# Kernel optimization log

Measured on AMD Instinct MI355X. Metric: run time of the kernel, lower is better.

## Reference

```python
import jax, jax.numpy as jnp
import numpy as np

N = 262144
HID = 200


def _lin_init(k, out_d, in_d):
    k1, k2 = jax.random.split(k)
    bound = 1.0 / np.sqrt(in_d)
    W = jax.random.uniform(k1, (out_d, in_d), minval=-bound, maxval=bound, dtype=jnp.float32)
    b = jax.random.uniform(k2, (out_d,), minval=-bound, maxval=bound, dtype=jnp.float32)
    return W, b


def setup_inputs() -> dict:
    key = jax.random.key(0)
    ks = jax.random.split(key, 10)
    Wu0, bu0 = _lin_init(ks[0], HID, 3)
    Wu1, bu1 = _lin_init(ks[1], HID, HID)
    Wu2, bu2 = _lin_init(ks[2], 1, HID)
    Wv0, bv0 = _lin_init(ks[3], HID, 3)
    Wv1, bv1 = _lin_init(ks[4], HID, HID)
    Wv2, bv2 = _lin_init(ks[5], 1, HID)
    Wf0, bf0 = _lin_init(ks[6], HID, 12)
    Wf1, bf1 = _lin_init(ks[7], HID, HID)
    Wf2, bf2 = _lin_init(ks[8], 2, HID)
    inputs = jax.random.normal(ks[9], (N, 3), dtype=jnp.float32)
    return dict(inputs=inputs,
                Wu0=Wu0, bu0=bu0, Wu1=Wu1, bu1=bu1, Wu2=Wu2, bu2=bu2,
                Wv0=Wv0, bv0=bv0, Wv1=Wv1, bv1=bv1, Wv2=Wv2, bv2=bv2,
                Wf0=Wf0, bf0=bf0, Wf1=Wf1, bf1=bf1, Wf2=Wf2, bf2=bf2)


def _mlp(x, W0, b0, W1, b1, W2, b2):
    # NN with num_layers=3: sin(Linear) -> sin(Linear) -> Linear
    h = jnp.sin(x @ W0.T + b0)
    h = jnp.sin(h @ W1.T + b1)
    return h @ W2.T + b2


def _scalar(pt, params):
    # per-point scalar network, pt: [3]
    W0, b0, W1, b1, W2, b2 = params
    h = jnp.sin(W0 @ pt + b0)
    h = jnp.sin(W1 @ h + b1)
    return (W2 @ h + b2)[0]


def _derivs(pt, params):
    # first derivatives (grad) and diagonal second derivatives u_xx, u_yy
    # via forward-over-reverse (jvp of grad) with unit tangents e_x, e_y.
    g = jax.grad(lambda p: _scalar(p, params))
    ex = jnp.array([1.0, 0.0, 0.0], dtype=pt.dtype)
    ey = jnp.array([0.0, 1.0, 0.0], dtype=pt.dtype)
    grad, hx = jax.jvp(g, (pt,), (ex,))
    _, hy = jax.jvp(g, (pt,), (ey,))
    return grad, hx[0], hy[1]


def _dhpm_forward(inputs, pu, pv, pf):
    u = _mlp(inputs, *pu)  # [N,1]
    v = _mlp(inputs, *pv)  # [N,1]
    gu, u_xx, u_yy = jax.vmap(lambda p: _derivs(p, pu))(inputs)
    gv, v_xx, v_yy = jax.vmap(lambda p: _derivs(p, pv))(inputs)
    u_x, u_y, u_t = gu[:, :1], gu[:, 1:2], gu[:, 2:3]
    v_x, v_y, v_t = gv[:, :1], gv[:, 1:2], gv[:, 2:3]
    u_xx = u_xx[:, None]; u_yy = u_yy[:, None]
    v_xx = v_xx[:, None]; v_yy = v_yy[:, None]
    feat = jnp.concatenate([u, v, u_t, v_t, u_x, u_xx, u_y, u_yy,
                            v_x, v_xx, v_y, v_yy], axis=1)  # [N,12]
    f = _mlp(feat, *pf)  # [N,2]
    return (u, v, u_t, v_t, u_x, u_xx, u_y, u_yy,
            v_x, v_xx, v_y, v_yy, f[:, :1], f[:, 1:])


def reference(inputs, Wu0, bu0, Wu1, bu1, Wu2, bu2,
              Wv0, bv0, Wv1, bv1, Wv2, bv2,
              Wf0, bf0, Wf1, bf1, Wf2, bf2):
    pu = (Wu0, bu0, Wu1, bu1, Wu2, bu2)
    pv = (Wv0, bv0, Wv1, bv1, Wv2, bv2)
    pf = (Wf0, bf0, Wf1, bf1, Wf2, bf2)
    return _dhpm_forward(inputs, pu, pv, pf)
```

## Files before the change

kernel.cpp:

```cpp
#include <hip/hip_runtime.h>


#define HID 200
#define NT 13
#define KT 7
#define BLDK 232
#define WCHUNK 8192
#define NTH 512
#define ELD 68

#define OFF_WU 0
#define OFF_WV 106496
#define OFF_WF 212992
#define OFF_CU 319488
#define OFF_CV 322688
#define OFF_CF 325888

typedef _Float16 f16;
typedef _Float16 f16x2 __attribute__((ext_vector_type(2)));
typedef _Float16 f16x8 __attribute__((ext_vector_type(8)));
typedef float f32x4 __attribute__((ext_vector_type(4)));

#define GLDS16(gp, lp) __builtin_amdgcn_global_load_lds( \
    (const __attribute__((address_space(1))) void*)(gp), \
    (__attribute__((address_space(3))) void*)(lp), 16, 0, 0)

__global__ __launch_bounds__(256) void dhpm_prep(
    const float* __restrict__ Wu1, const float* __restrict__ Wv1, const float* __restrict__ Wf1,
    const float* __restrict__ Wu0, const float* __restrict__ bu0,
    const float* __restrict__ Wv0, const float* __restrict__ bv0,
    const float* __restrict__ Wf0, const float* __restrict__ bf0,
    char* __restrict__ ws)
{
    int id = blockIdx.x * blockDim.x + threadIdx.x;
    const int nW = 3 * NT * 16 * 116;
    if (id < nW) {
        const int net = id / (NT*16*116);
        int e = id - net * (NT*16*116);
        const int nt  = e / (16*116);  e -= nt * (16*116);
        const int row = e / 116;
        const int k2  = e - row * 116;
        const int j   = nt*16 + row;
        const int k   = k2*2;
        const float* W = (net == 0) ? Wu1 : (net == 1) ? Wv1 : Wf1;
        f16x2 v; v[0] = (f16)0.f; v[1] = (f16)0.f;
        if (j < HID) {
            if (k     < HID) v[0] = (f16)W[j*HID + k];
            if (k + 1 < HID) v[1] = (f16)W[j*HID + k + 1];
        }
        *(f16x2*)(ws + net*106496 + nt*WCHUNK + row*464 + k2*4) = v;
        return;
    }
    id -= nW;
    if (id < 400) {
        const int net = id / HID;
        const int r   = id - net*HID;
        const float* W0 = net ? Wv0 : Wu0;
        const float* b0 = net ? bv0 : bu0;
        float4 c;
        c.x = W0[r*3+0]; c.y = W0[r*3+1]; c.z = W0[r*3+2]; c.w = b0[r];
        *(float4*)(ws + (net ? OFF_CV : OFF_CU) + r*16) = c;
        return;
    }
    id -= 400;
    if (id < HID) {
        const int i = id;
        float4 c0, c1, c2, c3;
        c0.x = Wf0[i*12+0];  c0.y = Wf0[i*12+1];  c0.z = Wf0[i*12+2];  c0.w = Wf0[i*12+3];
        c1.x = Wf0[i*12+4];  c1.y = Wf0[i*12+5];  c1.z = Wf0[i*12+6];  c1.w = Wf0[i*12+7];
        c2.x = Wf0[i*12+8];  c2.y = Wf0[i*12+9];  c2.z = Wf0[i*12+10]; c2.w = Wf0[i*12+11];
        c3.x = bf0[i]; c3.y = 0.f; c3.z = 0.f; c3.w = 0.f;
        char* p = ws + OFF_CF + i*64;
        *(float4*)(p)      = c0;
        *(float4*)(p + 16) = c1;
        *(float4*)(p + 32) = c2;
        *(float4*)(p + 48) = c3;
    }
}

__device__ __forceinline__ f32x4 mfma16(f16x8 a, f16x8 b, f32x4 c) {
    return __builtin_amdgcn_mfma_f32_16x16x32_f16(a, b, c, 0, 0, 0);
}

__device__ __forceinline__ void run_net(
    const float* __restrict__ inp, const char* __restrict__ ws,
    const int wOff, const int cstOff,
    const float* __restrict__ b1, const float* __restrict__ W2, const float b2s,
    const int cV, const int cXX, const int cYY,
    const int cX, const int cY, const int cT,
    char* __restrict__ Bb0, char* __restrict__ Bb1,
    float* __restrict__ exch, float* __restrict__ res,
    const int gp0, const int lane, const int w, const int q, const int g,
    const int jl, const int klo)
{
    const char* src = ws + wOff;

    GLDS16(src + w*1024 + lane*16, Bb0 + w*1024);

    f16x8 aP[3][KT];
    {
        const float4* cst = (const float4*)(ws + cstOff);
        const int pt = gp0 + q*16 + jl;
        const float x = inp[pt*3+0], y = inp[pt*3+1], tt = inp[pt*3+2];
        #pragma unroll
        for (int kt = 0; kt < KT; ++kt) {
            f16x8 f0, f1, f2;
            #pragma unroll
            for (int e = 0; e < 8; ++e) {
                const int i = kt*32 + klo*8 + e;
                const float4 c = cst[(i < HID) ? i : 0];
                const float z = fmaf(c.x, x, fmaf(c.y, y, fmaf(c.z, tt, c.w)));
                if (g == 0) {
                    const float s = __sinf(z);
                    f0[e] = (f16)s;
                    f1[e] = (f16)(-s * c.x * c.x);
                    f2[e] = (f16)(-s * c.y * c.y);
                } else {
                    const float cv = __cosf(z);
                    f0[e] = (f16)(cv * c.x);
                    f1[e] = (f16)(cv * c.y);
                    f2[e] = (f16)(cv * c.z);
                }
            }
            aP[0][kt] = f0; aP[1][kt] = f1; aP[2][kt] = f2;
        }
    }

    float p0a[4] = {0,0,0,0}, p1a[4] = {0,0,0,0}, p2a[4] = {0,0,0,0};

    float* E0  = exch;
    float* Edx = exch + 16*ELD;
    float* Edy = exch + 32*ELD;

    __syncthreads();

    for (int nt = 0; nt < NT; ++nt) {
        const char* Bcur = (nt & 1) ? Bb1 : Bb0;
        char*       Bnxt = (nt & 1) ? Bb0 : Bb1;
        if (nt + 1 < NT)
            GLDS16(src + (nt+1)*WCHUNK + w*1024 + lane*16, Bnxt + w*1024);

        f32x4 acc0 = {0,0,0,0}, acc1 = {0,0,0,0}, acc2 = {0,0,0,0};
        const f16* BH = (const f16*)Bcur;
        #pragma unroll
        for (int kt = 0; kt < KT; ++kt) {
            const f16x8 b = *(const f16x8*)&BH[jl*BLDK + kt*32 + klo*8];
            acc0 = mfma16(aP[0][kt], b, acc0);
            acc1 = mfma16(aP[1][kt], b, acc1);
            acc2 = mfma16(aP[2][kt], b, acc2);
        }

        const int j = nt*16 + jl;
        const float b1j = (j < HID) ? b1[j] : 0.f;
        const float w2j = (j < HID) ? W2[j] : 0.f;
        const int pcol = q*16 + klo*4;
        float wcr[4], wsr[4];
        if (g == 0) {
            f32x4 wc4;
            #pragma unroll
            for (int r = 0; r < 4; ++r) {
                float s1, c1;
                __sincosf(acc0[r] + b1j, &s1, &c1);
                wcr[r] = w2j * c1;
                wsr[r] = w2j * s1;
                p0a[r] += wsr[r];
                wc4[r] = wcr[r];
            }
            *(f32x4*)&E0[jl*ELD + pcol] = wc4;
        } else {
            *(f32x4*)&Edx[jl*ELD + pcol] = acc0;
            *(f32x4*)&Edy[jl*ELD + pcol] = acc1;
        }
        __syncthreads();

        if (g == 0) {
            const f32x4 ydx = *(const f32x4*)&Edx[jl*ELD + pcol];
            const f32x4 ydy = *(const f32x4*)&Edy[jl*ELD + pcol];
            #pragma unroll
            for (int r = 0; r < 4; ++r) {
                p1a[r] = fmaf(wcr[r], acc1[r], fmaf(-wsr[r]*ydx[r], ydx[r], p1a[r]));
                p2a[r] = fmaf(wcr[r], acc2[r], fmaf(-wsr[r]*ydy[r], ydy[r], p2a[r]));
            }
        } else {
            const f32x4 wc4 = *(const f32x4*)&E0[jl*ELD + pcol];
            #pragma unroll
            for (int r = 0; r < 4; ++r) {
                p0a[r] = fmaf(wc4[r], acc0[r], p0a[r]);
                p1a[r] = fmaf(wc4[r], acc1[r], p1a[r]);
                p2a[r] = fmaf(wc4[r], acc2[r], p2a[r]);
            }
        }
        __syncthreads();
    }

    #pragma unroll
    for (int d = 1; d < 16; d <<= 1)
        #pragma unroll
        for (int r = 0; r < 4; ++r) {
            p0a[r] += __shfl_xor(p0a[r], d);
            p1a[r] += __shfl_xor(p1a[r], d);
            p2a[r] += __shfl_xor(p2a[r], d);
        }
    if (jl == 0) {
        const int p0 = q*16 + klo*4;
        f32x4 v;
        if (g == 0) {
            #pragma unroll
            for (int r = 0; r < 4; ++r) v[r] = p0a[r] + b2s;
            *(f32x4*)&res[cV*72 + p0] = v;
            #pragma unroll
            for (int r = 0; r < 4; ++r) v[r] = p1a[r];
            *(f32x4*)&res[cXX*72 + p0] = v;
            #pragma unroll
            for (int r = 0; r < 4; ++r) v[r] = p2a[r];
            *(f32x4*)&res[cYY*72 + p0] = v;
        } else {
            #pragma unroll
            for (int r = 0; r < 4; ++r) v[r] = p0a[r];
            *(f32x4*)&res[cX*72 + p0] = v;
            #pragma unroll
            for (int r = 0; r < 4; ++r) v[r] = p1a[r];
            *(f32x4*)&res[cY*72 + p0] = v;
            #pragma unroll
            for (int r = 0; r < 4; ++r) v[r] = p2a[r];
            *(f32x4*)&res[cT*72 + p0] = v;
        }
    }
}

__global__ __launch_bounds__(NTH, 2) void dhpm_main(
    const float* __restrict__ inp, const char* __restrict__ ws,
    const float* __restrict__ bu1, const float* __restrict__ Wu2, const float* __restrict__ bu2,
    const float* __restrict__ bv1, const float* __restrict__ Wv2, const float* __restrict__ bv2,
    const float* __restrict__ bf1, const float* __restrict__ Wf2, const float* __restrict__ bf2,
    float* __restrict__ out, const int Np)
{
    __shared__ __align__(16) char LDS[37824];
    char*  Bb0  = LDS;
    char*  Bb1  = LDS + 8192;
    float* exch = (float*)(LDS + 16384);
    f16*   Af   = (f16*)LDS;
    float* res  = (float*)(LDS + 29696);
    float* pfb  = (float*)(LDS + 33728);

    const int t = threadIdx.x;
    const int lane = t & 63;
    const int w = __builtin_amdgcn_readfirstlane(t >> 6);
    const int q = w & 3, g = w >> 2;
    const int jl = lane & 15, klo = lane >> 4;
    const int gp0 = blockIdx.x * 64;

    run_net(inp, ws, OFF_WU, OFF_CU, bu1, Wu2, bu2[0], 0, 5, 7, 4, 6, 2,
            Bb0, Bb1, exch, res, gp0, lane, w, q, g, jl, klo);
    run_net(inp, ws, OFF_WV, OFF_CV, bv1, Wv2, bv2[0], 1, 9, 11, 8, 10, 3,
            Bb0, Bb1, exch, res, gp0, lane, w, q, g, jl, klo);

    __syncthreads();

    const int nown = (w < 5) ? 2 : 1;
    f16x8 bF[2][KT];
    #pragma unroll
    for (int ont = 0; ont < 2; ++ont)
        if (ont < nown) {
            const int nt = w + ont*8;
            #pragma unroll
            for (int kt = 0; kt < KT; ++kt)
                bF[ont][kt] = *(const f16x8*)(ws + OFF_WF + nt*WCHUNK
                                              + jl*464 + kt*64 + klo*16);
        }

    if (w < 4) {
        const int p = w*16 + jl;
        float fv[12];
        #pragma unroll
        for (int k = 0; k < 12; ++k) fv[k] = res[k*72 + p];
        const float4* cf = (const float4*)(ws + OFF_CF);
        #pragma unroll
        for (int kt = 0; kt < KT; ++kt) {
            f16x8 f;
            #pragma unroll
            for (int e = 0; e < 8; ++e) {
                const int i = kt*32 + klo*8 + e;
                const int ic = (i < HID) ? i : 0;
                const float4 c0 = cf[ic*4+0];
                const float4 c1 = cf[ic*4+1];
                const float4 c2 = cf[ic*4+2];
                const float4 c3 = cf[ic*4+3];
                float z = c3.x;
                z = fmaf(c0.x, fv[0], z);  z = fmaf(c0.y, fv[1], z);
                z = fmaf(c0.z, fv[2], z);  z = fmaf(c0.w, fv[3], z);
                z = fmaf(c1.x, fv[4], z);  z = fmaf(c1.y, fv[5], z);
                z = fmaf(c1.z, fv[6], z);  z = fmaf(c1.w, fv[7], z);
                z = fmaf(c2.x, fv[8], z);  z = fmaf(c2.y, fv[9], z);
                z = fmaf(c2.z, fv[10], z); z = fmaf(c2.w, fv[11], z);
                f[e] = (f16)__sinf(z);
            }
            *(f16x8*)((char*)Af + p*464 + kt*64 + klo*16) = f;
        }
    }
    __syncthreads();

    f32x4 accF[2][4];
    #pragma unroll
    for (int ont = 0; ont < 2; ++ont)
        #pragma unroll
        for (int mt = 0; mt < 4; ++mt) { f32x4 z = {0,0,0,0}; accF[ont][mt] = z; }

    #pragma unroll
    for (int kt = 0; kt < KT; ++kt)
        #pragma unroll
        for (int mt = 0; mt < 4; ++mt) {
            const f16x8 a = *(const f16x8*)((const char*)Af
                                + (mt*16 + jl)*464 + kt*64 + klo*16);
            #pragma unroll
            for (int ont = 0; ont < 2; ++ont)
                if (ont < nown)
                    accF[ont][mt] = mfma16(a, bF[ont][kt], accF[ont][mt]);
        }

    float pf0[4][4], pf1[4][4];
    #pragma unroll
    for (int mt = 0; mt < 4; ++mt)
        #pragma unroll
        for (int r = 0; r < 4; ++r) { pf0[mt][r] = 0.f; pf1[mt][r] = 0.f; }

    #pragma unroll
    for (int ont = 0; ont < 2; ++ont)
        if (ont < nown) {
            const int j = (w + ont*8)*16 + jl;
            const float bj = (j < HID) ? bf1[j] : 0.f;
            const float wa = (j < HID) ? Wf2[j] : 0.f;
            const float wb = (j < HID) ? Wf2[HID + j] : 0.f;
            #pragma unroll
            for (int mt = 0; mt < 4; ++mt)
                #pragma unroll
                for (int r = 0; r < 4; ++r) {
                    const float h = __sinf(accF[ont][mt][r] + bj);
                    pf0[mt][r] = fmaf(wa, h, pf0[mt][r]);
                    pf1[mt][r] = fmaf(wb, h, pf1[mt][r]);
                }
        }

    #pragma unroll
    for (int d = 1; d < 16; d <<= 1)
        #pragma unroll
        for (int mt = 0; mt < 4; ++mt)
            #pragma unroll
            for (int r = 0; r < 4; ++r) {
                pf0[mt][r] += __shfl_xor(pf0[mt][r], d);
                pf1[mt][r] += __shfl_xor(pf1[mt][r], d);
            }
    if (jl == 0) {
        #pragma unroll
        for (int mt = 0; mt < 4; ++mt) {
            f32x4 v0, v1;
            #pragma unroll
            for (int r = 0; r < 4; ++r) { v0[r] = pf0[mt][r]; v1[r] = pf1[mt][r]; }
            *(f32x4*)&pfb[w*128 + 0*64 + mt*16 + klo*4] = v0;
            *(f32x4*)&pfb[w*128 + 1*64 + mt*16 + klo*4] = v1;
        }
    }
    __syncthreads();
    if (t < 128) {
        const int pt = t & 63, ch = t >> 6;
        float s = bf2[ch];
        #pragma unroll
        for (int ww = 0; ww < 8; ++ww) s += pfb[ww*128 + ch*64 + pt];
        res[(12 + ch)*72 + pt] = s;
    }
    __syncthreads();

    for (int e = t; e < 14*64; e += NTH) {
        const int c = e >> 6, p = e & 63;
        out[(size_t)c*Np + gp0 + p] = res[c*72 + p];
    }
}

extern "C" void kernel_launch(void* const* d_in, const int* in_sizes, int n_in,
                              void* d_out, int out_size, void* d_ws, size_t ws_size,
                              hipStream_t stream) {
    const float* inp = (const float*)d_in[0];
    const float* Wu0 = (const float*)d_in[1];  const float* bu0 = (const float*)d_in[2];
    const float* Wu1 = (const float*)d_in[3];  const float* bu1 = (const float*)d_in[4];
    const float* Wu2 = (const float*)d_in[5];  const float* bu2 = (const float*)d_in[6];
    const float* Wv0 = (const float*)d_in[7];  const float* bv0 = (const float*)d_in[8];
    const float* Wv1 = (const float*)d_in[9];  const float* bv1 = (const float*)d_in[10];
    const float* Wv2 = (const float*)d_in[11]; const float* bv2 = (const float*)d_in[12];
    const float* Wf0 = (const float*)d_in[13]; const float* bf0 = (const float*)d_in[14];
    const float* Wf1 = (const float*)d_in[15]; const float* bf1 = (const float*)d_in[16];
    const float* Wf2 = (const float*)d_in[17]; const float* bf2 = (const float*)d_in[18];
    float* out = (float*)d_out;
    char* ws = (char*)d_ws;

    const int Np = in_sizes[0] / 3;

    const int nTot = 3*NT*16*116 + 400 + HID;
    dhpm_prep<<<(nTot + 255) / 256, 256, 0, stream>>>(
        Wu1, Wv1, Wf1, Wu0, bu0, Wv0, bv0, Wf0, bf0, ws);
    dhpm_main<<<Np / 64, NTH, 0, stream>>>(
        inp, ws, bu1, Wu2, bu2, bv1, Wv2, bv2, bf1, Wf2, bf2, out, Np);
}
```

Measured before the change: 718.3 us.

## Double-buffer exchange to drop one barrier per tile and restructure Hessian accumulation

Each tile iteration now has a single barrier instead of two. The exchange buffers are double-buffered (EA/EB alternate by tile parity). The group-1 waves compute the -w*s*y^2 second-derivative terms themselves from the exchanged sin values, and the results are merged into res after the loop with an extra barrier. Layer-0 constants now include precomputed -a^2 terms, and the b1/W2 loads are prefetched one tile ahead. Launch bounds are raised to 4 blocks per SM, which tightens the register limit and risks spills.

```diff
diff --git a/kernel.cpp b/kernel.cpp
--- a/kernel.cpp
+++ b/kernel.cpp
@@ -13,8 +13,8 @@
 #define OFF_WV 106496
 #define OFF_WF 212992
 #define OFF_CU 319488
-#define OFF_CV 322688
-#define OFF_CF 325888
+#define OFF_CV 325888
+#define OFF_CF 332288
 
 typedef _Float16 f16;
 typedef _Float16 f16x2 __attribute__((ext_vector_type(2)));
@@ -57,9 +57,13 @@
         const int r   = id - net*HID;
         const float* W0 = net ? Wv0 : Wu0;
         const float* b0 = net ? bv0 : bu0;
-        float4 c;
-        c.x = W0[r*3+0]; c.y = W0[r*3+1]; c.z = W0[r*3+2]; c.w = b0[r];
-        *(float4*)(ws + (net ? OFF_CV : OFF_CU) + r*16) = c;
+        const float ax = W0[r*3+0], ay = W0[r*3+1], at = W0[r*3+2];
+        float4 c0, c1;
+        c0.x = ax; c0.y = ay; c0.z = at; c0.w = b0[r];
+        c1.x = -ax*ax; c1.y = -ay*ay; c1.z = 0.f; c1.w = 0.f;
+        char* p = ws + (net ? OFF_CV : OFF_CU) + r*32;
+        *(float4*)(p)      = c0;
+        *(float4*)(p + 16) = c1;
         return;
     }
     id -= 400;
@@ -108,13 +112,15 @@
             #pragma unroll
             for (int e = 0; e < 8; ++e) {
                 const int i = kt*32 + klo*8 + e;
-                const float4 c = cst[(i < HID) ? i : 0];
+                const int ic = (i < HID) ? i : 0;
+                const float4 c = cst[ic*2];
                 const float z = fmaf(c.x, x, fmaf(c.y, y, fmaf(c.z, tt, c.w)));
                 if (g == 0) {
+                    const float4 c2 = cst[ic*2+1];
                     const float s = __sinf(z);
                     f0[e] = (f16)s;
-                    f1[e] = (f16)(-s * c.x * c.x);
-                    f2[e] = (f16)(-s * c.y * c.y);
+                    f1[e] = (f16)(s * c2.x);
+                    f2[e] = (f16)(s * c2.y);
                 } else {
                     const float cv = __cosf(z);
                     f0[e] = (f16)(cv * c.x);
@@ -127,10 +133,15 @@
     }
 
     float p0a[4] = {0,0,0,0}, p1a[4] = {0,0,0,0}, p2a[4] = {0,0,0,0};
-
-    float* E0  = exch;
-    float* Edx = exch + 16*ELD;
-    float* Edy = exch + 32*ELD;
+    float p3a[4] = {0,0,0,0}, p4a[4] = {0,0,0,0};
+
+    float* EA0 = exch;
+    float* EA1 = exch + 16*ELD;
+    float* EB0 = exch + 32*ELD;
+    float* EB1 = exch + 48*ELD;
+
+    float bj_n = 0.f, wj_n = 0.f;
+    if (g == 0) { bj_n = b1[jl]; wj_n = W2[jl]; }
 
     __syncthreads();
 
@@ -140,6 +151,13 @@
         if (nt + 1 < NT)
             GLDS16(src + (nt+1)*WCHUNK + w*1024 + lane*16, Bnxt + w*1024);
 
+        const float bj = bj_n, wj = wj_n;
+        if (g == 0 && nt + 1 < NT) {
+            const int j2 = (nt+1)*16 + jl;
+            bj_n = (j2 < HID) ? b1[j2] : 0.f;
+            wj_n = (j2 < HID) ? W2[j2] : 0.f;
+        }
+
         f32x4 acc0 = {0,0,0,0}, acc1 = {0,0,0,0}, acc2 = {0,0,0,0};
         const f16* BH = (const f16*)Bcur;
         #pragma unroll
@@ -150,59 +168,56 @@
             acc2 = mfma16(aP[2][kt], b, acc2);
         }
 
-        const int j = nt*16 + jl;
-        const float b1j = (j < HID) ? b1[j] : 0.f;
-        const float w2j = (j < HID) ? W2[j] : 0.f;
         const int pcol = q*16 + klo*4;
-        float wcr[4], wsr[4];
+        float* EA = (nt & 1) ? EA1 : EA0;
+        float* EB = (nt & 1) ? EB1 : EB0;
         if (g == 0) {
-            f32x4 wc4;
+            f32x4 wc4, ws4;
             #pragma unroll
             for (int r = 0; r < 4; ++r) {
                 float s1, c1;
-                __sincosf(acc0[r] + b1j, &s1, &c1);
-                wcr[r] = w2j * c1;
-                wsr[r] = w2j * s1;
-                p0a[r] += wsr[r];
-                wc4[r] = wcr[r];
-            }
-            *(f32x4*)&E0[jl*ELD + pcol] = wc4;
-        } else {
-            *(f32x4*)&Edx[jl*ELD + pcol] = acc0;
-            *(f32x4*)&Edy[jl*ELD + pcol] = acc1;
+                __sincosf(acc0[r] + bj, &s1, &c1);
+                wc4[r] = wj * c1;
+                ws4[r] = wj * s1;
+                p0a[r] += ws4[r];
+                p1a[r] = fmaf(wc4[r], acc1[r], p1a[r]);
+                p2a[r] = fmaf(wc4[r], acc2[r], p2a[r]);
+            }
+            *(f32x4*)&EA[jl*ELD + pcol] = wc4;
+            *(f32x4*)&EB[jl*ELD + pcol] = ws4;
         }
         __syncthreads();
-
-        if (g == 0) {
-            const f32x4 ydx = *(const f32x4*)&Edx[jl*ELD + pcol];
-            const f32x4 ydy = *(const f32x4*)&Edy[jl*ELD + pcol];
-            #pragma unroll
-            for (int r = 0; r < 4; ++r) {
-                p1a[r] = fmaf(wcr[r], acc1[r], fmaf(-wsr[r]*ydx[r], ydx[r], p1a[r]));
-                p2a[r] = fmaf(wcr[r], acc2[r], fmaf(-wsr[r]*ydy[r], ydy[r], p2a[r]));
-            }
-        } else {
-            const f32x4 wc4 = *(const f32x4*)&E0[jl*ELD + pcol];
+        if (g == 1) {
+            const f32x4 wc4 = *(const f32x4*)&EA[jl*ELD + pcol];
+            const f32x4 ws4 = *(const f32x4*)&EB[jl*ELD + pcol];
             #pragma unroll
             for (int r = 0; r < 4; ++r) {
                 p0a[r] = fmaf(wc4[r], acc0[r], p0a[r]);
                 p1a[r] = fmaf(wc4[r], acc1[r], p1a[r]);
                 p2a[r] = fmaf(wc4[r], acc2[r], p2a[r]);
-            }
-        }
-        __syncthreads();
-    }
-
-    #pragma unroll
-    for (int d = 1; d < 16; d <<= 1)
+                p3a[r] = fmaf(ws4[r]*acc0[r], acc0[r], p3a[r]);
+                p4a[r] = fmaf(ws4[r]*acc1[r], acc1[r], p4a[r]);
+            }
+        }
+    }
+
+    #pragma unroll
+    for (int d = 1; d < 16; d <<= 1) {
         #pragma unroll
         for (int r = 0; r < 4; ++r) {
             p0a[r] += __shfl_xor(p0a[r], d);
             p1a[r] += __shfl_xor(p1a[r], d);
             p2a[r] += __shfl_xor(p2a[r], d);
         }
+        if (g == 1)
+            #pragma unroll
+            for (int r = 0; r < 4; ++r) {
+                p3a[r] += __shfl_xor(p3a[r], d);
+                p4a[r] += __shfl_xor(p4a[r], d);
+            }
+    }
+    const int p0 = q*16 + klo*4;
     if (jl == 0) {
-        const int p0 = q*16 + klo*4;
         f32x4 v;
         if (g == 0) {
             #pragma unroll
@@ -226,22 +241,31 @@
             *(f32x4*)&res[cT*72 + p0] = v;
         }
     }
+    __syncthreads();
+    if (g == 1 && jl == 0) {
+        f32x4 a = *(const f32x4*)&res[cXX*72 + p0];
+        f32x4 b = *(const f32x4*)&res[cYY*72 + p0];
+        #pragma unroll
+        for (int r = 0; r < 4; ++r) { a[r] -= p3a[r]; b[r] -= p4a[r]; }
+        *(f32x4*)&res[cXX*72 + p0] = a;
+        *(f32x4*)&res[cYY*72 + p0] = b;
+    }
 }
 
-__global__ __launch_bounds__(NTH, 2) void dhpm_main(
+__global__ __launch_bounds__(NTH, 4) void dhpm_main(
     const float* __restrict__ inp, const char* __restrict__ ws,
     const float* __restrict__ bu1, const float* __restrict__ Wu2, const float* __restrict__ bu2,
     const float* __restrict__ bv1, const float* __restrict__ Wv2, const float* __restrict__ bv2,
     const float* __restrict__ bf1, const float* __restrict__ Wf2, const float* __restrict__ bf2,
     float* __restrict__ out, const int Np)
 {
-    __shared__ __align__(16) char LDS[37824];
+    __shared__ __align__(16) char LDS[41920];
     char*  Bb0  = LDS;
     char*  Bb1  = LDS + 8192;
     float* exch = (float*)(LDS + 16384);
     f16*   Af   = (f16*)LDS;
-    float* res  = (float*)(LDS + 29696);
-    float* pfb  = (float*)(LDS + 33728);
+    float* res  = (float*)(LDS + 33792);
+    float* pfb  = (float*)(LDS + 37824);
 
     const int t = threadIdx.x;
     const int lane = t & 63;
```

New measurement: 1.231 ms. +71.4%, slower.
